# Kernel optimization log

Hardware: AMD Instinct MI355X
Metric: run time of the kernel (lower is better)

Reference implementation:

```python
import jax, jax.numpy as jnp
import numpy as np

P = 8  # patch size
EPS = 1e-5

def ln_ch(x, w, b):
    # WithBias LayerNorm over channel dim of (B,C,H,W): torch code flattens to (B,HW,C) and norms last dim
    mu = x.mean(axis=1, keepdims=True)
    var = ((x - mu) ** 2).mean(axis=1, keepdims=True)
    return (x - mu) / jnp.sqrt(var + EPS) * w[None, :, None, None] + b[None, :, None, None]

def conv1x1(x, w):
    # w: [C_out, C_in]
    return jnp.einsum('bchw,oc->bohw', x, w)

def dwconv3x3(x, w):
    # depthwise 3x3, w: [C,1,3,3]
    return jax.lax.conv_general_dilated(x, w, (1, 1), 'SAME', dimension_numbers=('NCHW', 'OIHW', 'NCHW'), feature_group_count=x.shape[1])

def patchify(x):
    b, c, H, W = x.shape
    return x.reshape(b, c, H // P, P, W // P, P).transpose(0, 1, 2, 4, 3, 5)  # b c h w p1 p2

def unpatchify(x):
    b, c, h, w, p1, p2 = x.shape
    return x.transpose(0, 1, 2, 4, 3, 5).reshape(b, c, h * p1, w * p2)

def setup_inputs() -> dict:
    key = jax.random.key(0)
    ks = jax.random.split(key, 16)
    B, C, H, W = 4, 64, 256, 256
    hid = 2 * C  # ffn_expansion_factor=2
    s = 0.02
    return {
        'x': jax.random.normal(ks[0], (B, C, H, W), jnp.float32),
        'evt': jax.random.normal(ks[1], (B, C, H, W), jnp.float32),
        'ln1i_w': jnp.ones((C,), jnp.float32), 'ln1i_b': jnp.zeros((C,), jnp.float32),
        'ln1e_w': jnp.ones((C,), jnp.float32), 'ln1e_b': jnp.zeros((C,), jnp.float32),
        'w_q': jax.random.normal(ks[2], (2 * C, C), jnp.float32) * s,
        'dw_q': jax.random.normal(ks[3], (2 * C, 1, 3, 3), jnp.float32) * s,
        'w_kv': jax.random.normal(ks[4], (4 * C, C), jnp.float32) * s,
        'dw_kv': jax.random.normal(ks[5], (4 * C, 1, 3, 3), jnp.float32) * s,
        'lnA_w': jnp.ones((2 * C,), jnp.float32), 'lnA_b': jnp.zeros((2 * C,), jnp.float32),
        'w_po_attn': jax.random.normal(ks[6], (C, 2 * C), jnp.float32) * s,
        'ln2_w': jnp.ones((C,), jnp.float32), 'ln2_b': jnp.zeros((C,), jnp.float32),
        'w_pi': jax.random.normal(ks[7], (2 * hid, C), jnp.float32) * s,
        'fft_param': jnp.ones((2 * hid, 1, 1, P, P // 2 + 1), jnp.float32),
        'dw_ffn': jax.random.normal(ks[8], (2 * hid, 1, 3, 3), jnp.float32) * s,
        'w_po_ffn': jax.random.normal(ks[9], (C, hid), jnp.float32) * s,
    }

def reference(x, evt, ln1i_w, ln1i_b, ln1e_w, ln1e_b, w_q, dw_q, w_kv, dw_kv, lnA_w, lnA_b, w_po_attn, ln2_w, ln2_b, w_pi, fft_param, dw_ffn, w_po_ffn):
    # ---- EventFSAS cross attention ----
    xn = ln_ch(x, ln1i_w, ln1i_b)
    en = ln_ch(evt, ln1e_w, ln1e_b)
    q = dwconv3x3(conv1x1(xn, w_q), dw_q)               # (B,2C,H,W)
    kv = dwconv3x3(conv1x1(en, w_kv), dw_kv)            # (B,4C,H,W)
    k, v = jnp.split(kv, 2, axis=1)
    qf = jnp.fft.rfft2(patchify(q))                      # (B,2C,h,w,8,5) complex
    kf = jnp.fft.rfft2(patchify(k))
    out = jnp.fft.irfft2(qf * kf, s=(P, P))
    out = ln_ch(unpatchify(out), lnA_w, lnA_b)
    x = x + conv1x1(v * out, w_po_attn)
    # ---- DFFN ----
    y = conv1x1(ln_ch(x, ln2_w, ln2_b), w_pi)            # (B,4C,H,W)
    yf = jnp.fft.rfft2(patchify(y)) * fft_param
    y = unpatchify(jnp.fft.irfft2(yf, s=(P, P)))
    y = dwconv3x3(y, dw_ffn)
    y1, y2 = jnp.split(y, 2, axis=1)
    y = jax.nn.gelu(y1, approximate=False) * y2          # torch nn.GELU is exact erf form
    return x + conv1x1(y, w_po_ffn)
```

## Files before the change

### kernel.cpp

```cpp
#include <hip/hip_runtime.h>

#define HW 65536
#define NPOS 262144

typedef unsigned int   u32;
typedef unsigned short u16;
typedef __attribute__((ext_vector_type(8))) short v8s;
typedef __attribute__((ext_vector_type(4))) float f32x4;
typedef __attribute__((ext_vector_type(2))) float f32x2;

__device__ __forceinline__ float bf2f(u16 h){
  union { u32 u; float f; } c; c.u = ((u32)h) << 16; return c.f;
}
__device__ __forceinline__ u16 f2bf(float f){
  union { u32 u; float f; } c; c.f = f;
  u32 r = c.u + 0x7fffu + ((c.u >> 16) & 1u);
  return (u16)(r >> 16);
}
__device__ __forceinline__ u32 pk2(float a, float b){
  return (u32)f2bf(a) | ((u32)f2bf(b) << 16);
}
__device__ __forceinline__ v8s as8(uint4 u){
  union { uint4 a; v8s b; } c; c.a = u; return c.b;
}
__device__ __forceinline__ f32x2 up2(u32 u){
  union { u32 u; float f; } lo, hi;
  lo.u = u << 16; hi.u = u & 0xffff0000u;
  f32x2 r; r.x = lo.f; r.y = hi.f; return r;
}
__device__ __forceinline__ float gelu_exact(float x){
  return 0.5f*x*(1.0f+erff(x*0.70710678118654752f));
}

__device__ void fold_w(const float* __restrict__ W, int rows,
                       const float* __restrict__ lw, const float* __restrict__ lb,
                       u16* __restrict__ Wf, float* __restrict__ A, float* __restrict__ B){
  int tid = threadIdx.x;
  for (int e = tid; e < rows*64; e += 256) Wf[e] = f2bf(lw[e & 63] * W[e]);
  for (int r = tid; r < rows; r += 256){
    float a = 0.f, b2 = 0.f;
    for (int c = 0; c < 64; c++){ float w = W[r*64+c]; a += lw[c]*w; b2 += lb[c]*w; }
    A[r] = a; B[r] = b2;
  }
}

__global__ void k_prep(const float* __restrict__ M, float* __restrict__ g,
    const float* wq,  const float* l1iw, const float* l1ib, u16* wqf,  float* aq,  float* bq,
    const float* wkv, const float* l1ew, const float* l1eb, u16* wkvf, float* akv, float* bkv,
    const float* wpi, const float* l2w,  const float* l2b,  u16* wpif, float* api, float* bpi,
    const float* wpa, u16* wpaf, const float* wpf, u16* wpff)
{
  int blk = blockIdx.x, tid = threadIdx.x;
  if (blk < 64){
    int t = blk*256 + tid;
    int c = t >> 6, uv = t & 63, u = uv >> 3, v = uv & 7;
    const float* mc = M + c*40;
    const float ctab[8] = {1.f, 0.70710678118654752f, 0.f, -0.70710678118654752f,
                           -1.f, -0.70710678118654752f, 0.f, 0.70710678118654752f};
    float acc = 0.f;
    for (int k1=0;k1<8;k1++)
      for (int k2=0;k2<8;k2++){
        float s = (k2<=4) ? mc[k1*5+k2] : mc[(((8-k1)&7)*5) + (8-k2)];
        acc += s * ctab[(k1*u + k2*v)&7];
      }
    g[t] = acc * (1.f/64.f);
  } else if (blk == 64){ fold_w(wq, 128, l1iw, l1ib, wqf, aq, bq); }
  else if (blk == 65){ fold_w(wkv, 256, l1ew, l1eb, wkvf, akv, bkv); }
  else if (blk == 66){ fold_w(wpi, 256, l2w, l2b, wpif, api, bpi); }
  else if (blk == 67){ for (int e=tid; e<64*128; e+=256) wpaf[e] = f2bf(wpa[e]); }
  else               { for (int e=tid; e<64*128; e+=256) wpff[e] = f2bf(wpf[e]); }
}

__global__ void k_prep2(const float* __restrict__ g, u16* __restrict__ CM){
  int c = blockIdx.x;
  const float* gc = g + (size_t)c*64;
  u16* cm = CM + (size_t)c*4096;
  for (int e = threadIdx.x; e < 4096; e += 256){
    int o = e >> 6, i = e & 63;
    int du = ((o>>3) - (i>>3)) & 7, dv = ((o&7) - (i&7)) & 7;
    cm[e] = f2bf(gc[du*8 + dv]);
  }
}

struct GA {
  const float* src; const u16* Wf; const float* Af; const float* Bf;
  u32* dst; int o0; int dstOffP; int Cdp; int b0; int pxbase;
};

template<int NZ>
__global__ __launch_bounds__(256) void k_gemm64(GA a0, GA a1){
  GA a = (blockIdx.y == 0) ? a0 : a1;
  __shared__ uint4 lsX[128*8];
  __shared__ uint4 lsW[64*NZ*8];
  __shared__ float2 sPart[256];
  __shared__ float2 sStat[128];
  int tid = threadIdx.x;
  int px = tid & 127, hf = tid >> 7;
  int p0 = a.pxbase + blockIdx.x*128;
  int b = p0 >> 16, hwb = p0 & 65535;
  {
    const uint4* wsrc = (const uint4*)(a.Wf + (size_t)a.o0*64);
    #pragma unroll
    for (int i=0; i<NZ*2; i++){
      int idx = i*256 + tid, row = idx>>3, s = idx&7;
      lsW[row*8 + (s ^ (row&7))] = wsrc[idx];
    }
  }
  {
    const float* sp = a.src + (size_t)b*64*HW + hwb + px + (size_t)(hf*32)*HW;
    float e[32];
    #pragma unroll
    for (int c=0;c<32;c++) e[c] = sp[(size_t)c*HW];
    float sm = 0.f, sq = 0.f;
    #pragma unroll
    for (int c=0;c<32;c++){ sm += e[c]; sq += e[c]*e[c]; }
    uint4* xrow = lsX + px*8;
    #pragma unroll
    for (int sl=0; sl<4; sl++){
      uint4 pkv;
      pkv.x = pk2(e[sl*8+0], e[sl*8+1]); pkv.y = pk2(e[sl*8+2], e[sl*8+3]);
      pkv.z = pk2(e[sl*8+4], e[sl*8+5]); pkv.w = pk2(e[sl*8+6], e[sl*8+7]);
      xrow[(hf*4+sl) ^ (px&7)] = pkv;
    }
    sPart[tid] = make_float2(sm, sq);
  }
  __syncthreads();
  if (tid < 128){
    float2 A = sPart[tid], B = sPart[tid+128];
    float s = A.x + B.x, q = A.y + B.y;
    float mu = s*(1.f/64.f);
    float var = q*(1.f/64.f) - mu*mu;
    sStat[tid] = make_float2(mu, rsqrtf(fmaxf(var,0.f)+1e-5f));
  }
  __syncthreads();
  int w = tid>>6, l = tid&63, g = l>>4, c15 = l&15;
  float2 stv[2];
  #pragma unroll
  for (int pp=0;pp<2;pp++) stv[pp] = sStat[w*32 + pp*16 + c15];

  #pragma unroll
  for (int z=0; z<NZ; z++){
    f32x4 acc[2][4];
    #pragma unroll
    for (int pp=0;pp<2;pp++)
      #pragma unroll
      for (int po=0;po<4;po++) acc[pp][po] = (f32x4){0.f,0.f,0.f,0.f};
    #pragma unroll
    for (int kk=0; kk<2; kk++){
      v8s wf[4], xf[2];
      #pragma unroll
      for (int po=0;po<4;po++){ int row = z*64 + po*16 + c15; wf[po] = as8(lsW[row*8 + ((kk*4+g) ^ (row&7))]); }
      #pragma unroll
      for (int pp=0;pp<2;pp++){ int row = w*32 + pp*16 + c15; xf[pp] = as8(lsX[row*8 + ((kk*4+g) ^ (row&7))]); }
      #pragma unroll
      for (int pp=0;pp<2;pp++)
        #pragma unroll
        for (int po=0;po<4;po++)
          acc[pp][po] = __builtin_amdgcn_mfma_f32_16x16x32_bf16(wf[po], xf[pp], acc[pp][po], 0,0,0);
    }
    size_t obaseP = ((size_t)(b - a.b0)*a.Cdp + a.dstOffP + z*32)*HW + hwb + w*32;
    #pragma unroll
    for (int po=0;po<4;po++)
      #pragma unroll
      for (int j2=0;j2<2;j2++){
        int oc = po*16 + g*4 + j2*2;
        float A0 = a.Af[a.o0 + z*64 + oc],   B0 = a.Bf[a.o0 + z*64 + oc];
        float A1 = a.Af[a.o0 + z*64 + oc+1], B1 = a.Bf[a.o0 + z*64 + oc+1];
        int ocp = po*8 + g*2 + j2;
        u32* dp = a.dst + obaseP + (size_t)ocp*HW + c15;
        #pragma unroll
        for (int pp=0;pp<2;pp++){
          float lo = stv[pp].y*(acc[pp][po][j2*2  ] - stv[pp].x*A0) + B0;
          float hi = stv[pp].y*(acc[pp][po][j2*2+1] - stv[pp].x*A1) + B1;
          dp[pp*16] = pk2(lo, hi);
        }
      }
  }
}

__global__ __launch_bounds__(256) void k_gemm_attn(
    const float* __restrict__ x, const u32* __restrict__ orawp, const u32* __restrict__ vbp,
    const float* __restrict__ lnw, const float* __restrict__ lnb,
    const u16* __restrict__ Wf, float* __restrict__ out)
{
  __shared__ uint4 lsX[128*16];
  __shared__ uint4 lsW[64*16];
  __shared__ float2 sPart[256];
  __shared__ float2 sStat[128];
  int tid = threadIdx.x;
  int p0 = blockIdx.x*128;
  int b = p0 >> 16, hwb = p0 & 65535;
  int px = tid & 127, hf = tid >> 7;
  {
    const uint4* wsrc = (const uint4*)Wf;
    #pragma unroll
    for (int i=0;i<4;i++){
      int idx = i*256 + tid, row = idx>>4, s = idx&15;
      lsW[row*16 + (s ^ (row&15))] = wsrc[idx];
    }
  }
  const u32* orp = orawp + ((size_t)b*64 + hf*32)*HW + hwb + px;
  {
    u32 r32[32];
    #pragma unroll
    for (int i=0;i<32;i++) r32[i] = orp[(size_t)i*HW];
    float sum = 0.f, ssq = 0.f;
    #pragma unroll
    for (int sl=0; sl<8; sl++){
      u32 wds[4];
      #pragma unroll
      for (int q2=0;q2<4;q2++){
        u32 wv = r32[sl*4+q2];
        float fl = bf2f((u16)(wv&0xffff)), fh = bf2f((u16)(wv>>16));
        sum += fl + fh; ssq += fl*fl + fh*fh;
        wds[q2] = wv;
      }
      int s = hf*8 + sl;
      lsX[px*16 + (s ^ (px&15))] = make_uint4(wds[0],wds[1],wds[2],wds[3]);
    }
    sPart[tid] = make_float2(sum, ssq);
  }
  __syncthreads();
  if (tid < 128){
    float2 A = sPart[tid], B = sPart[tid+128];
    float s = A.x + B.x, q = A.y + B.y;
    float mu = s*(1.f/128.f);
    float var = q*(1.f/128.f) - mu*mu;
    sStat[tid] = make_float2(mu, rsqrtf(fmaxf(var,0.f)+1e-5f));
  }
  __syncthreads();
  {
    float2 st = sStat[px];
    const u32* vp = vbp + ((size_t)b*64 + hf*32)*HW + hwb + px;
    u32 v32[32];
    #pragma unroll
    for (int i=0;i<32;i++) v32[i] = vp[(size_t)i*HW];
    #pragma unroll
    for (int sl=0; sl<8; sl++){
      int s = hf*8 + sl;
      int li = px*16 + (s ^ (px&15));
      uint4 raw = lsX[li];
      u32 wds[4] = {raw.x, raw.y, raw.z, raw.w};
      u32 ow[4];
      #pragma unroll
      for (int q2=0;q2<4;q2++){
        int ch = hf*64 + sl*8 + q2*2;
        float e0 = bf2f((u16)(wds[q2]&0xffff)), e1 = bf2f((u16)(wds[q2]>>16));
        u32 vv = v32[sl*4+q2];
        float v0 = bf2f((u16)(vv&0xffff)), v1 = bf2f((u16)(vv>>16));
        float r0 = ((e0-st.x)*st.y*lnw[ch  ] + lnb[ch  ])*v0;
        float r1 = ((e1-st.x)*st.y*lnw[ch+1] + lnb[ch+1])*v1;
        ow[q2] = pk2(r0, r1);
      }
      lsX[li] = make_uint4(ow[0],ow[1],ow[2],ow[3]);
    }
  }
  __syncthreads();
  int w4 = tid>>6, l = tid&63, g = l>>4, c15 = l&15;
  f32x4 acc[2][4];
  #pragma unroll
  for (int pp=0;pp<2;pp++)
    #pragma unroll
    for (int po=0;po<4;po++) acc[pp][po] = (f32x4){0.f,0.f,0.f,0.f};
  #pragma unroll
  for (int kk=0; kk<4; kk++){
    v8s wf[4], xf[2];
    #pragma unroll
    for (int po=0;po<4;po++){ int row = po*16 + c15; wf[po] = as8(lsW[row*16 + ((kk*4+g) ^ (row&15))]); }
    #pragma unroll
    for (int pp=0;pp<2;pp++){ int row = w4*32 + pp*16 + c15; xf[pp] = as8(lsX[row*16 + ((kk*4+g) ^ (row&15))]); }
    #pragma unroll
    for (int pp=0;pp<2;pp++)
      #pragma unroll
      for (int po=0;po<4;po++)
        acc[pp][po] = __builtin_amdgcn_mfma_f32_16x16x32_bf16(wf[po], xf[pp], acc[pp][po], 0,0,0);
  }
  size_t obase = (size_t)b*64*HW + hwb + w4*32;
  #pragma unroll
  for (int po=0;po<4;po++)
    #pragma unroll
    for (int j=0;j<4;j++){
      int oc = po*16 + g*4 + j;
      const float* xs = x + obase + (size_t)oc*HW + c15;
      float* dp = out + obase + (size_t)oc*HW + c15;
      #pragma unroll
      for (int pp=0;pp<2;pp++) dp[pp*16] = xs[pp*16] + acc[pp][po][j];
    }
}

__global__ __launch_bounds__(256) void k_gemm_ffn(
    const u32* __restrict__ y3gp, const u16* __restrict__ Wf, float* __restrict__ out,
    int pxbase, int b0)
{
  __shared__ uint4 lsX[128*16];
  __shared__ uint4 lsW[64*16];
  int tid = threadIdx.x;
  int p0 = pxbase + blockIdx.x*128;
  int b = p0 >> 16, hwb = p0 & 65535;
  int px = tid & 127, hf = tid >> 7;
  {
    const uint4* wsrc = (const uint4*)Wf;
    #pragma unroll
    for (int i=0;i<4;i++){
      int idx = i*256 + tid, row = idx>>4, s = idx&15;
      lsW[row*16 + (s ^ (row&15))] = wsrc[idx];
    }
  }
  const u32* yp = y3gp + ((size_t)(b-b0)*64 + hf*32)*HW + hwb + px;
  {
    u32 r32[32];
    #pragma unroll
    for (int i=0;i<32;i++) r32[i] = yp[(size_t)i*HW];
    #pragma unroll
    for (int sl=0; sl<8; sl++){
      int s = hf*8 + sl;
      lsX[px*16 + (s ^ (px&15))] = make_uint4(r32[sl*4+0],r32[sl*4+1],r32[sl*4+2],r32[sl*4+3]);
    }
  }
  __syncthreads();
  int w4 = tid>>6, l = tid&63, g = l>>4, c15 = l&15;
  f32x4 acc[2][4];
  #pragma unroll
  for (int pp=0;pp<2;pp++)
    #pragma unroll
    for (int po=0;po<4;po++) acc[pp][po] = (f32x4){0.f,0.f,0.f,0.f};
  #pragma unroll
  for (int kk=0; kk<4; kk++){
    v8s wf[4], xf[2];
    #pragma unroll
    for (int po=0;po<4;po++){ int row = po*16 + c15; wf[po] = as8(lsW[row*16 + ((kk*4+g) ^ (row&15))]); }
    #pragma unroll
    for (int pp=0;pp<2;pp++){ int row = w4*32 + pp*16 + c15; xf[pp] = as8(lsX[row*16 + ((kk*4+g) ^ (row&15))]); }
    #pragma unroll
    for (int pp=0;pp<2;pp++)
      #pragma unroll
      for (int po=0;po<4;po++)
        acc[pp][po] = __builtin_amdgcn_mfma_f32_16x16x32_bf16(wf[po], xf[pp], acc[pp][po], 0,0,0);
  }
  size_t obase = (size_t)b*64*HW + hwb + w4*32;
  #pragma unroll
  for (int po=0;po<4;po++)
    #pragma unroll
    for (int j=0;j<4;j++){
      int oc = po*16 + g*4 + j;
      float* dp = out + obase + (size_t)oc*HW + c15;
      #pragma unroll
      for (int pp=0;pp<2;pp++) dp[pp*16] = dp[pp*16] + acc[pp][po][j];
    }
}

__device__ __forceinline__ void dw8p_acc2(const u32* __restrict__ sp,
    const float* __restrict__ w9lo, const float* __restrict__ w9hi,
    int h, int w8, f32x2 a2[8])
{
  #pragma unroll
  for (int r=0;r<3;r++){
    int hh = h + r - 1;
    if (hh < 0 || hh > 255) continue;
    const u32* rp = sp + hh*256 + w8;
    uint4 ua = *(const uint4*)rp;
    uint4 ub = *(const uint4*)(rp+4);
    u32 e[8] = {ua.x,ua.y,ua.z,ua.w,ub.x,ub.y,ub.z,ub.w};
    u32 lef = (w8 > 0)   ? rp[-1] : 0u;
    u32 rig = (w8 < 248) ? rp[8]  : 0u;
    f32x2 vm[10];
    vm[0] = up2(lef);
    #pragma unroll
    for (int j=0;j<8;j++) vm[j+1] = up2(e[j]);
    vm[9] = up2(rig);
    f32x2 wa = {w9lo[r*3  ], w9hi[r*3  ]};
    f32x2 wb = {w9lo[r*3+1], w9hi[r*3+1]};
    f32x2 wc = {w9lo[r*3+2], w9hi[r*3+2]};
    #pragma unroll
    for (int j=0;j<8;j++)
      a2[j] += vm[j]*wa + vm[j+1]*wb + vm[j+2]*wc;
  }
}

__global__ __launch_bounds__(256) void k_dw8p(
    const u32* __restrict__ src, const float* __restrict__ wgt, int c0,
    u32* __restrict__ dstp, int dstOffP, int prMask, int prShift)
{
  int t = blockIdx.x*256 + threadIdx.x;
  int w8 = (t & 31)*8, h = (t>>5) & 255;
  int plane = t >> 13;
  int pr = plane & prMask, b = plane >> prShift;
  const u32* sp = src + (size_t)plane*HW;
  const float* w9 = wgt + (size_t)(c0 + 2*pr)*9;
  f32x2 a2[8];
  #pragma unroll
  for (int j=0;j<8;j++) a2[j] = (f32x2){0.f,0.f};
  dw8p_acc2(sp, w9, w9+9, h, w8, a2);
  u32* dp = dstp + ((size_t)(b*64 + dstOffP + pr))*HW + h*256 + w8;
  uint4 s0, s1;
  s0.x=pk2(a2[0].x,a2[0].y); s0.y=pk2(a2[1].x,a2[1].y); s0.z=pk2(a2[2].x,a2[2].y); s0.w=pk2(a2[3].x,a2[3].y);
  s1.x=pk2(a2[4].x,a2[4].y); s1.y=pk2(a2[5].x,a2[5].y); s1.z=pk2(a2[6].x,a2[6].y); s1.w=pk2(a2[7].x,a2[7].y);
  *(uint4*)dp = s0; *(uint4*)(dp+4) = s1;
}

__global__ __launch_bounds__(256) void k_dw8gp(
    const u32* __restrict__ Y0p, const float* __restrict__ wgt, u32* __restrict__ Y3gp)
{
  int t = blockIdx.x*256 + threadIdx.x;
  int w8 = (t & 31)*8, h = (t>>5) & 255;
  int pc = t >> 13;
  int pr = pc & 63, bl = pc >> 6;
  const u32* spA = Y0p + ((size_t)(bl*128 + pr))*HW;
  const u32* spG = Y0p + ((size_t)(bl*128 + 64 + pr))*HW;
  const float* w9a = wgt + (size_t)(2*pr)*9;
  const float* w9g = wgt + (size_t)(128 + 2*pr)*9;
  f32x2 aA[8], aG[8];
  #pragma unroll
  for (int j=0;j<8;j++){ aA[j] = (f32x2){0.f,0.f}; aG[j] = (f32x2){0.f,0.f}; }
  dw8p_acc2(spA, w9a, w9a+9, h, w8, aA);
  dw8p_acc2(spG, w9g, w9g+9, h, w8, aG);
  u32* dp = Y3gp + ((size_t)(bl*64 + pr))*HW + h*256 + w8;
  uint4 s0, s1;
  s0.x=pk2(gelu_exact(aA[0].x)*aG[0].x, gelu_exact(aA[0].y)*aG[0].y);
  s0.y=pk2(gelu_exact(aA[1].x)*aG[1].x, gelu_exact(aA[1].y)*aG[1].y);
  s0.z=pk2(gelu_exact(aA[2].x)*aG[2].x, gelu_exact(aA[2].y)*aG[2].y);
  s0.w=pk2(gelu_exact(aA[3].x)*aG[3].x, gelu_exact(aA[3].y)*aG[3].y);
  s1.x=pk2(gelu_exact(aA[4].x)*aG[4].x, gelu_exact(aA[4].y)*aG[4].y);
  s1.y=pk2(gelu_exact(aA[5].x)*aG[5].x, gelu_exact(aA[5].y)*aG[5].y);
  s1.z=pk2(gelu_exact(aA[6].x)*aG[6].x, gelu_exact(aA[6].y)*aG[6].y);
  s1.w=pk2(gelu_exact(aA[7].x)*aG[7].x, gelu_exact(aA[7].y)*aG[7].y);
  *(uint4*)dp = s0; *(uint4*)(dp+4) = s1;
}

__global__ __launch_bounds__(256) void k_circqk4(
    const u32* __restrict__ bq, const u32* __restrict__ bk,
    const float* __restrict__ dwq, const float* __restrict__ dwk, int c0,
    u32* __restrict__ orawp, int oprBase, int cpb)
{
  __shared__ f32x2 qd[8][288];
  __shared__ f32x2 kd[8][288];
  int tid = threadIdx.x;
  int p = tid & 31, i = tid >> 5;
  int pr = blockIdx.y, b = blockIdx.z;
  int h0 = blockIdx.x*8;
  const u32* qp = bq + ((size_t)(b*cpb+pr))*HW;
  const u32* kp = bk + ((size_t)(b*cpb+pr))*HW;
  const float* wq9 = dwq + (size_t)(c0 + 2*pr)*9;
  const float* wk9 = dwk + (size_t)(c0 + 2*pr)*9;
  {
    f32x2 a2[8];
    #pragma unroll
    for (int j=0;j<8;j++) a2[j] = (f32x2){0.f,0.f};
    dw8p_acc2(qp, wq9, wq9+9, h0+i, p*8, a2);
    #pragma unroll
    for (int j=0;j<8;j++) qd[i][p*9+j] = a2[j];
  }
  {
    f32x2 a2[8];
    #pragma unroll
    for (int j=0;j<8;j++) a2[j] = (f32x2){0.f,0.f};
    dw8p_acc2(kp, wk9, wk9+9, h0+i, p*8, a2);
    #pragma unroll
    for (int j=0;j<8;j++) kd[i][p*9+j] = a2[j];
  }
  __syncthreads();
  f32x2 o[8];
  #pragma unroll
  for (int j=0;j<8;j++) o[j] = (f32x2){0.f,0.f};
  #pragma unroll
  for (int u=0;u<8;u++){
    int ku = (i-u)&7;
    f32x2 qv[8], kr[8];
    #pragma unroll
    for (int v=0;v<8;v++) qv[v] = qd[u][p*9+v];
    #pragma unroll
    for (int e=0;e<8;e++) kr[e] = kd[ku][p*9+e];
    #pragma unroll
    for (int v=0;v<8;v++){
      f32x2 qq = qv[v];
      #pragma unroll
      for (int j=0;j<8;j++)
        o[j] += qq * kr[(j-v)&7];
    }
  }
  u32* op = orawp + ((size_t)(b*64 + oprBase + pr))*HW + (size_t)(h0+i)*256 + p*8;
  uint4 s0, s1;
  s0.x=pk2(o[0].x,o[0].y); s0.y=pk2(o[1].x,o[1].y); s0.z=pk2(o[2].x,o[2].y); s0.w=pk2(o[3].x,o[3].y);
  s1.x=pk2(o[4].x,o[4].y); s1.y=pk2(o[5].x,o[5].y); s1.z=pk2(o[6].x,o[6].y); s1.w=pk2(o[7].x,o[7].y);
  *(uint4*)op = s0; *(uint4*)(op+4) = s1;
}

__global__ __launch_bounds__(256) void k_circg_mfma(
    u32* __restrict__ y, const u16* __restrict__ CM)
{
  __shared__ uint4 lsA[2][64*8];
  __shared__ uint4 lsB[2][64*8];
  int tid = threadIdx.x;
  int pr = blockIdx.y, b = blockIdx.z;
  int h0 = blockIdx.x*16;
  u32* plane = y + ((size_t)(b*128+pr))*HW;
  {
    const uint4* cmsrc = (const uint4*)(CM + (size_t)(2*pr)*4096);
    #pragma unroll
    for (int t=0; t<4; t++){
      int idx = t*256 + tid;
      int ch = idx >> 9, e = idx & 511;
      int row = e >> 3, s = e & 7;
      lsA[ch][row*8 + (s ^ (row&7))] = cmsrc[ch*512 + e];
    }
  }
  {
    #pragma unroll
    for (int t=0; t<2; t++){
      int rr = t*256 + tid;
      int n = rr >> 3, i = rr & 7;
      const u32* rp = plane + (size_t)(h0 + (n>>5)*8 + i)*256 + (n&31)*8;
      uint4 ua = *(const uint4*)rp;
      uint4 ub = *(const uint4*)(rp+4);
      u32 e[8] = {ua.x,ua.y,ua.z,ua.w,ub.x,ub.y,ub.z,ub.w};
      uint4 L, H;
      L.x = (e[0]&0xffffu) | (e[1]<<16);
      L.y = (e[2]&0xffffu) | (e[3]<<16);
      L.z = (e[4]&0xffffu) | (e[5]<<16);
      L.w = (e[6]&0xffffu) | (e[7]<<16);
      H.x = (e[0]>>16) | (e[1]&0xffff0000u);
      H.y = (e[2]>>16) | (e[3]&0xffff0000u);
      H.z = (e[4]>>16) | (e[5]&0xffff0000u);
      H.w = (e[6]>>16) | (e[7]&0xffff0000u);
      lsB[0][n*8 + (i ^ (n&7))] = L;
      lsB[1][n*8 + (i ^ (n&7))] = H;
    }
  }
  __syncthreads();
  int w = tid>>6, l = tid&63, g = l>>4, c15 = l&15;
  f32x4 acc[2][4];
  #pragma unroll
  for (int ch=0;ch<2;ch++)
    #pragma unroll
    for (int po=0;po<4;po++) acc[ch][po] = (f32x4){0.f,0.f,0.f,0.f};
  #pragma unroll
  for (int kk=0; kk<2; kk++){
    v8s bfr[2];
    { int row = w*16 + c15;
      bfr[0] = as8(lsB[0][row*8 + ((kk*4+g) ^ (row&7))]);
      bfr[1] = as8(lsB[1][row*8 + ((kk*4+g) ^ (row&7))]); }
    #pragma unroll
    for (int po=0;po<4;po++){
      int row = po*16 + c15;
      v8s aL = as8(lsA[0][row*8 + ((kk*4+g) ^ (row&7))]);
      v8s aH = as8(lsA[1][row*8 + ((kk*4+g) ^ (row&7))]);
      acc[0][po] = __builtin_amdgcn_mfma_f32_16x16x32_bf16(aL, bfr[0], acc[0][po], 0,0,0);
      acc[1][po] = __builtin_amdgcn_mfma_f32_16x16x32_bf16(aH, bfr[1], acc[1][po], 0,0,0);
    }
  }
  int patch = w*16 + c15;
  u32* pbase = plane + (size_t)(h0 + (patch>>5)*8)*256 + (patch&31)*8;
  #pragma unroll
  for (int po=0;po<4;po++){
    int oh = po*2 + (g>>1), ow4 = 4*(g&1);
    uint4 sv;
    sv.x = pk2(acc[0][po][0], acc[1][po][0]);
    sv.y = pk2(acc[0][po][1], acc[1][po][1]);
    sv.z = pk2(acc[0][po][2], acc[1][po][2]);
    sv.w = pk2(acc[0][po][3], acc[1][po][3]);
    *(uint4*)(pbase + (size_t)oh*256 + ow4) = sv;
  }
}

extern "C" void kernel_launch(void* const* d_in, const int* in_sizes, int n_in,
                              void* d_out, int out_size, void* d_ws, size_t ws_size,
                              hipStream_t stream)
{
  const float* x       = (const float*)d_in[0];
  const float* evt     = (const float*)d_in[1];
  const float* ln1i_w  = (const float*)d_in[2];
  const float* ln1i_b  = (const float*)d_in[3];
  const float* ln1e_w  = (const float*)d_in[4];
  const float* ln1e_b  = (const float*)d_in[5];
  const float* w_q     = (const float*)d_in[6];
  const float* dw_q    = (const float*)d_in[7];
  const float* w_kv    = (const float*)d_in[8];
  const float* dw_kv   = (const float*)d_in[9];
  const float* lnA_w   = (const float*)d_in[10];
  const float* lnA_b   = (const float*)d_in[11];
  const float* w_po_at = (const float*)d_in[12];
  const float* ln2_w   = (const float*)d_in[13];
  const float* ln2_b   = (const float*)d_in[14];
  const float* w_pi    = (const float*)d_in[15];
  const float* fft_par = (const float*)d_in[16];
  const float* dw_ffn  = (const float*)d_in[17];
  const float* w_poffn = (const float*)d_in[18];
  float* out = (float*)d_out;

  char* ws = (char*)d_ws;
  const size_t MiB = 1048576ull;
  bool big = (ws_size >= 200*MiB);
  size_t smOff = big ? 192*MiB : 160*MiB;
  char* sm = ws + smOff;
  float* G    = (float*)(sm);
  u16* WQF    = (u16*)(sm + 65536);
  u16* WKVF   = (u16*)(sm + 81920);
  u16* WPIF   = (u16*)(sm + 114688);
  u16* WPAF   = (u16*)(sm + 147456);
  u16* WPFF   = (u16*)(sm + 163840);
  float* AQ   = (float*)(sm + 180224);
  float* BQ   = (float*)(sm + 180736);
  float* AKV  = (float*)(sm + 181248);
  float* BKV  = (float*)(sm + 182272);
  float* API  = (float*)(sm + 183296);
  float* BPI  = (float*)(sm + 184320);
  u16* CMAT   = (u16*)(sm + 1*MiB);

  dim3 blk256(256);

  k_prep<<<69, blk256, 0, stream>>>(fft_par, G,
      w_q, ln1i_w, ln1i_b, WQF, AQ, BQ,
      w_kv, ln1e_w, ln1e_b, WKVF, AKV, BKV,
      w_pi, ln2_w, ln2_b, WPIF, API, BPI,
      w_po_at, WPAF, w_poffn, WPFF);
  k_prep2<<<256, blk256, 0, stream>>>(G, CMAT);

  if (big){
    u32* QBUF  = (u32*)(ws);
    u32* KBUF  = (u32*)(ws + 64*MiB);
    u32* ORAWp = (u32*)(ws + 128*MiB);
    u32* PV    = (u32*)(ws + 64*MiB);
    u32* VBUFp = (u32*)(ws);
    u32* Y0p   = (u32*)(ws);
    u32* Y3Gp  = (u32*)(ws + 128*MiB);

    GA qa = {x,   WQF,  AQ,  BQ,  QBUF, 0, 0, 64, 0, 0};
    GA ka = {evt, WKVF, AKV, BKV, KBUF, 0, 0, 64, 0, 0};
    k_gemm64<2><<<dim3(2048,2,1), blk256, 0, stream>>>(qa, ka);
    k_circqk4<<<dim3(32,64,4), blk256, 0, stream>>>(QBUF, KBUF, dw_q, dw_kv, 0, ORAWp, 0, 64);
    GA va = {evt, WKVF, AKV, BKV, PV, 128, 0, 64, 0, 0};
    k_gemm64<2><<<dim3(2048,1,1), blk256, 0, stream>>>(va, va);
    k_dw8p<<<8192, blk256, 0, stream>>>(PV, dw_kv, 128, VBUFp, 0, 63, 6);
    k_gemm_attn<<<2048, blk256, 0, stream>>>(x, ORAWp, VBUFp, lnA_w, lnA_b, WPAF, out);
    GA pa = {out, WPIF, API, BPI, Y0p, 0, 0, 128, 0, 0};
    k_gemm64<4><<<dim3(2048,1,1), blk256, 0, stream>>>(pa, pa);
    k_circg_mfma<<<dim3(16,128,4), blk256, 0, stream>>>(Y0p, CMAT);
    k_dw8gp<<<8192, blk256, 0, stream>>>(Y0p, dw_ffn, Y3Gp);
    k_gemm_ffn<<<2048, blk256, 0, stream>>>(Y3Gp, WPFF, out, 0, 0);
  } else {
    u32* P1p   = (u32*)(ws);
    u32* ORAWp = (u32*)(ws + 32*MiB);
    u32* P2p   = (u32*)(ws + 96*MiB);
    u32* VBUFp = (u32*)(ws + 96*MiB);
    u32* Y0p   = (u32*)(ws);
    u32* Y3Gp  = (u32*)(ws + 64*MiB);

    for (int i=0;i<2;i++){
      GA qa = {x,   WQF,  AQ,  BQ,  P1p, 64*i, 0, 32, 0, 0};
      GA ka = {evt, WKVF, AKV, BKV, P2p, 64*i, 0, 32, 0, 0};
      k_gemm64<1><<<dim3(2048,2,1), blk256, 0, stream>>>(qa, ka);
      k_circqk4<<<dim3(32,32,4), blk256, 0, stream>>>(P1p, P2p, dw_q, dw_kv, 64*i, ORAWp, 32*i, 32);
    }
    for (int i=0;i<2;i++){
      GA va = {evt, WKVF, AKV, BKV, P1p, 128+64*i, 0, 32, 0, 0};
      k_gemm64<1><<<dim3(2048,1,1), blk256, 0, stream>>>(va, va);
      k_dw8p<<<4096, blk256, 0, stream>>>(P1p, dw_kv, 128+64*i, VBUFp, 32*i, 31, 5);
    }
    k_gemm_attn<<<2048, blk256, 0, stream>>>(x, ORAWp, VBUFp, lnA_w, lnA_b, WPAF, out);
    for (int h=0;h<2;h++){
      GA pa = {out, WPIF, API, BPI, Y0p, 0, 0, 128, 2*h, h*131072};
      k_gemm64<4><<<dim3(1024,1,1), blk256, 0, stream>>>(pa, pa);
      k_circg_mfma<<<dim3(16,128,2), blk256, 0, stream>>>(Y0p, CMAT);
      k_dw8gp<<<4096, blk256, 0, stream>>>(Y0p, dw_ffn, Y3Gp);
      k_gemm_ffn<<<1024, blk256, 0, stream>>>(Y3Gp, WPFF, out, h*131072, 2*h);
    }
  }
}
```

Baseline: 462.4 us.

## Fuse V-projection GEMM with circular QK kernel into one heterogeneous launch

Merges the V 1x1-conv GEMM and the per-patch circular Q·K correlation into a single kernel, where one block in five runs the GEMM and the rest run the circulant work. The V projection output is staged in the output buffer so it no longer aliases the K buffer that the circulant blocks are still reading. The aim is to overlap the memory-bound GEMM with the compute-heavy circulant work and remove one launch plus the tail bubble between them. It also adds stride parameters to the dwconv and circqk kernels, and in exchange brings branch-divergent block roles and a shared-memory footprint sized for the larger path.

```diff
diff --git a/kernel.cpp b/kernel.cpp
--- a/kernel.cpp
+++ b/kernel.cpp
@@ -178,177 +178,6 @@
   }
 }
 
-__global__ __launch_bounds__(256) void k_gemm_attn(
-    const float* __restrict__ x, const u32* __restrict__ orawp, const u32* __restrict__ vbp,
-    const float* __restrict__ lnw, const float* __restrict__ lnb,
-    const u16* __restrict__ Wf, float* __restrict__ out)
-{
-  __shared__ uint4 lsX[128*16];
-  __shared__ uint4 lsW[64*16];
-  __shared__ float2 sPart[256];
-  __shared__ float2 sStat[128];
-  int tid = threadIdx.x;
-  int p0 = blockIdx.x*128;
-  int b = p0 >> 16, hwb = p0 & 65535;
-  int px = tid & 127, hf = tid >> 7;
-  {
-    const uint4* wsrc = (const uint4*)Wf;
-    #pragma unroll
-    for (int i=0;i<4;i++){
-      int idx = i*256 + tid, row = idx>>4, s = idx&15;
-      lsW[row*16 + (s ^ (row&15))] = wsrc[idx];
-    }
-  }
-  const u32* orp = orawp + ((size_t)b*64 + hf*32)*HW + hwb + px;
-  {
-    u32 r32[32];
-    #pragma unroll
-    for (int i=0;i<32;i++) r32[i] = orp[(size_t)i*HW];
-    float sum = 0.f, ssq = 0.f;
-    #pragma unroll
-    for (int sl=0; sl<8; sl++){
-      u32 wds[4];
-      #pragma unroll
-      for (int q2=0;q2<4;q2++){
-        u32 wv = r32[sl*4+q2];
-        float fl = bf2f((u16)(wv&0xffff)), fh = bf2f((u16)(wv>>16));
-        sum += fl + fh; ssq += fl*fl + fh*fh;
-        wds[q2] = wv;
-      }
-      int s = hf*8 + sl;
-      lsX[px*16 + (s ^ (px&15))] = make_uint4(wds[0],wds[1],wds[2],wds[3]);
-    }
-    sPart[tid] = make_float2(sum, ssq);
-  }
-  __syncthreads();
-  if (tid < 128){
-    float2 A = sPart[tid], B = sPart[tid+128];
-    float s = A.x + B.x, q = A.y + B.y;
-    float mu = s*(1.f/128.f);
-    float var = q*(1.f/128.f) - mu*mu;
-    sStat[tid] = make_float2(mu, rsqrtf(fmaxf(var,0.f)+1e-5f));
-  }
-  __syncthreads();
-  {
-    float2 st = sStat[px];
-    const u32* vp = vbp + ((size_t)b*64 + hf*32)*HW + hwb + px;
-    u32 v32[32];
-    #pragma unroll
-    for (int i=0;i<32;i++) v32[i] = vp[(size_t)i*HW];
-    #pragma unroll
-    for (int sl=0; sl<8; sl++){
-      int s = hf*8 + sl;
-      int li = px*16 + (s ^ (px&15));
-      uint4 raw = lsX[li];
-      u32 wds[4] = {raw.x, raw.y, raw.z, raw.w};
-      u32 ow[4];
-      #pragma unroll
-      for (int q2=0;q2<4;q2++){
-        int ch = hf*64 + sl*8 + q2*2;
-        float e0 = bf2f((u16)(wds[q2]&0xffff)), e1 = bf2f((u16)(wds[q2]>>16));
-        u32 vv = v32[sl*4+q2];
-        float v0 = bf2f((u16)(vv&0xffff)), v1 = bf2f((u16)(vv>>16));
-        float r0 = ((e0-st.x)*st.y*lnw[ch  ] + lnb[ch  ])*v0;
-        float r1 = ((e1-st.x)*st.y*lnw[ch+1] + lnb[ch+1])*v1;
-        ow[q2] = pk2(r0, r1);
-      }
-      lsX[li] = make_uint4(ow[0],ow[1],ow[2],ow[3]);
-    }
-  }
-  __syncthreads();
-  int w4 = tid>>6, l = tid&63, g = l>>4, c15 = l&15;
-  f32x4 acc[2][4];
-  #pragma unroll
-  for (int pp=0;pp<2;pp++)
-    #pragma unroll
-    for (int po=0;po<4;po++) acc[pp][po] = (f32x4){0.f,0.f,0.f,0.f};
-  #pragma unroll
-  for (int kk=0; kk<4; kk++){
-    v8s wf[4], xf[2];
-    #pragma unroll
-    for (int po=0;po<4;po++){ int row = po*16 + c15; wf[po] = as8(lsW[row*16 + ((kk*4+g) ^ (row&15))]); }
-    #pragma unroll
-    for (int pp=0;pp<2;pp++){ int row = w4*32 + pp*16 + c15; xf[pp] = as8(lsX[row*16 + ((kk*4+g) ^ (row&15))]); }
-    #pragma unroll
-    for (int pp=0;pp<2;pp++)
-      #pragma unroll
-      for (int po=0;po<4;po++)
-        acc[pp][po] = __builtin_amdgcn_mfma_f32_16x16x32_bf16(wf[po], xf[pp], acc[pp][po], 0,0,0);
-  }
-  size_t obase = (size_t)b*64*HW + hwb + w4*32;
-  #pragma unroll
-  for (int po=0;po<4;po++)
-    #pragma unroll
-    for (int j=0;j<4;j++){
-      int oc = po*16 + g*4 + j;
-      const float* xs = x + obase + (size_t)oc*HW + c15;
-      float* dp = out + obase + (size_t)oc*HW + c15;
-      #pragma unroll
-      for (int pp=0;pp<2;pp++) dp[pp*16] = xs[pp*16] + acc[pp][po][j];
-    }
-}
-
-__global__ __launch_bounds__(256) void k_gemm_ffn(
-    const u32* __restrict__ y3gp, const u16* __restrict__ Wf, float* __restrict__ out,
-    int pxbase, int b0)
-{
-  __shared__ uint4 lsX[128*16];
-  __shared__ uint4 lsW[64*16];
-  int tid = threadIdx.x;
-  int p0 = pxbase + blockIdx.x*128;
-  int b = p0 >> 16, hwb = p0 & 65535;
-  int px = tid & 127, hf = tid >> 7;
-  {
-    const uint4* wsrc = (const uint4*)Wf;
-    #pragma unroll
-    for (int i=0;i<4;i++){
-      int idx = i*256 + tid, row = idx>>4, s = idx&15;
-      lsW[row*16 + (s ^ (row&15))] = wsrc[idx];
-    }
-  }
-  const u32* yp = y3gp + ((size_t)(b-b0)*64 + hf*32)*HW + hwb + px;
-  {
-    u32 r32[32];
-    #pragma unroll
-    for (int i=0;i<32;i++) r32[i] = yp[(size_t)i*HW];
-    #pragma unroll
-    for (int sl=0; sl<8; sl++){
-      int s = hf*8 + sl;
-      lsX[px*16 + (s ^ (px&15))] = make_uint4(r32[sl*4+0],r32[sl*4+1],r32[sl*4+2],r32[sl*4+3]);
-    }
-  }
-  __syncthreads();
-  int w4 = tid>>6, l = tid&63, g = l>>4, c15 = l&15;
-  f32x4 acc[2][4];
-  #pragma unroll
-  for (int pp=0;pp<2;pp++)
-    #pragma unroll
-    for (int po=0;po<4;po++) acc[pp][po] = (f32x4){0.f,0.f,0.f,0.f};
-  #pragma unroll
-  for (int kk=0; kk<4; kk++){
-    v8s wf[4], xf[2];
-    #pragma unroll
-    for (int po=0;po<4;po++){ int row = po*16 + c15; wf[po] = as8(lsW[row*16 + ((kk*4+g) ^ (row&15))]); }
-    #pragma unroll
-    for (int pp=0;pp<2;pp++){ int row = w4*32 + pp*16 + c15; xf[pp] = as8(lsX[row*16 + ((kk*4+g) ^ (row&15))]); }
-    #pragma unroll
-    for (int pp=0;pp<2;pp++)
-      #pragma unroll
-      for (int po=0;po<4;po++)
-        acc[pp][po] = __builtin_amdgcn_mfma_f32_16x16x32_bf16(wf[po], xf[pp], acc[pp][po], 0,0,0);
-  }
-  size_t obase = (size_t)b*64*HW + hwb + w4*32;
-  #pragma unroll
-  for (int po=0;po<4;po++)
-    #pragma unroll
-    for (int j=0;j<4;j++){
-      int oc = po*16 + g*4 + j;
-      float* dp = out + obase + (size_t)oc*HW + c15;
-      #pragma unroll
-      for (int pp=0;pp<2;pp++) dp[pp*16] = dp[pp*16] + acc[pp][po][j];
-    }
-}
-
 __device__ __forceinline__ void dw8p_acc2(const u32* __restrict__ sp,
     const float* __restrict__ w9lo, const float* __restrict__ w9hi,
     int h, int w8, f32x2 a2[8])
@@ -377,15 +206,338 @@
   }
 }
 
+__global__ __launch_bounds__(256) void k_fused_cv(
+    const u32* __restrict__ bq, const u32* __restrict__ bk,
+    const float* __restrict__ dwq, const float* __restrict__ dwk,
+    u32* __restrict__ orawp,
+    const float* __restrict__ vsrc, const u16* __restrict__ Wf,
+    const float* __restrict__ Af, const float* __restrict__ Bf,
+    u32* __restrict__ vdst)
+{
+  __shared__ uint4 smemq[2304];
+  int bid = blockIdx.x;
+  int tid = threadIdx.x;
+  if (bid % 5 == 0){
+    int gb = bid / 5;
+    uint4* lsX = smemq;
+    uint4* lsW = smemq + 1024;
+    float2* sPart = (float2*)(smemq + 2048);
+    float2* sStat = (float2*)((char*)(smemq + 2048) + 2048);
+    int px = tid & 127, hf = tid >> 7;
+    int p0 = gb*128;
+    int b = p0 >> 16, hwb = p0 & 65535;
+    {
+      const uint4* wsrc = (const uint4*)(Wf + (size_t)128*64);
+      #pragma unroll
+      for (int i=0; i<4; i++){
+        int idx = i*256 + tid, row = idx>>3, s = idx&7;
+        lsW[row*8 + (s ^ (row&7))] = wsrc[idx];
+      }
+    }
+    {
+      const float* sp = vsrc + (size_t)b*64*HW + hwb + px + (size_t)(hf*32)*HW;
+      float e[32];
+      #pragma unroll
+      for (int c=0;c<32;c++) e[c] = sp[(size_t)c*HW];
+      float sm = 0.f, sq = 0.f;
+      #pragma unroll
+      for (int c=0;c<32;c++){ sm += e[c]; sq += e[c]*e[c]; }
+      uint4* xrow = lsX + px*8;
+      #pragma unroll
+      for (int sl=0; sl<4; sl++){
+        uint4 pkv;
+        pkv.x = pk2(e[sl*8+0], e[sl*8+1]); pkv.y = pk2(e[sl*8+2], e[sl*8+3]);
+        pkv.z = pk2(e[sl*8+4], e[sl*8+5]); pkv.w = pk2(e[sl*8+6], e[sl*8+7]);
+        xrow[(hf*4+sl) ^ (px&7)] = pkv;
+      }
+      sPart[tid] = make_float2(sm, sq);
+    }
+    __syncthreads();
+    if (tid < 128){
+      float2 A = sPart[tid], B = sPart[tid+128];
+      float s = A.x + B.x, q = A.y + B.y;
+      float mu = s*(1.f/64.f);
+      float var = q*(1.f/64.f) - mu*mu;
+      sStat[tid] = make_float2(mu, rsqrtf(fmaxf(var,0.f)+1e-5f));
+    }
+    __syncthreads();
+    int w = tid>>6, l = tid&63, g = l>>4, c15 = l&15;
+    float2 stv[2];
+    #pragma unroll
+    for (int pp=0;pp<2;pp++) stv[pp] = sStat[w*32 + pp*16 + c15];
+    #pragma unroll
+    for (int z=0; z<2; z++){
+      f32x4 acc[2][4];
+      #pragma unroll
+      for (int pp=0;pp<2;pp++)
+        #pragma unroll
+        for (int po=0;po<4;po++) acc[pp][po] = (f32x4){0.f,0.f,0.f,0.f};
+      #pragma unroll
+      for (int kk=0; kk<2; kk++){
+        v8s wf[4], xf[2];
+        #pragma unroll
+        for (int po=0;po<4;po++){ int row = z*64 + po*16 + c15; wf[po] = as8(lsW[row*8 + ((kk*4+g) ^ (row&7))]); }
+        #pragma unroll
+        for (int pp=0;pp<2;pp++){ int row = w*32 + pp*16 + c15; xf[pp] = as8(lsX[row*8 + ((kk*4+g) ^ (row&7))]); }
+        #pragma unroll
+        for (int pp=0;pp<2;pp++)
+          #pragma unroll
+          for (int po=0;po<4;po++)
+            acc[pp][po] = __builtin_amdgcn_mfma_f32_16x16x32_bf16(wf[po], xf[pp], acc[pp][po], 0,0,0);
+      }
+      size_t obaseP = ((size_t)b*64 + z*32)*HW + hwb + w*32;
+      #pragma unroll
+      for (int po=0;po<4;po++)
+        #pragma unroll
+        for (int j2=0;j2<2;j2++){
+          int oc = po*16 + g*4 + j2*2;
+          float A0 = Af[128 + z*64 + oc],   B0 = Bf[128 + z*64 + oc];
+          float A1 = Af[128 + z*64 + oc+1], B1 = Bf[128 + z*64 + oc+1];
+          int ocp = po*8 + g*2 + j2;
+          u32* dp = vdst + obaseP + (size_t)ocp*HW + c15;
+          #pragma unroll
+          for (int pp=0;pp<2;pp++){
+            float lo = stv[pp].y*(acc[pp][po][j2*2  ] - stv[pp].x*A0) + B0;
+            float hi = stv[pp].y*(acc[pp][po][j2*2+1] - stv[pp].x*A1) + B1;
+            dp[pp*16] = pk2(lo, hi);
+          }
+        }
+    }
+  } else {
+    int cq = bid - bid/5 - 1;
+    int strip = cq & 31, pr = (cq >> 5) & 63, b = cq >> 11;
+    f32x2 (*qd)[288] = (f32x2(*)[288])smemq;
+    f32x2 (*kd)[288] = (f32x2(*)[288])((char*)smemq + 18432);
+    int p = tid & 31, i = tid >> 5;
+    int h0 = strip*8;
+    const u32* qp = bq + ((size_t)(b*64+pr))*HW;
+    const u32* kp = bk + ((size_t)(b*64+pr))*HW;
+    const float* wq9 = dwq + (size_t)(2*pr)*9;
+    const float* wk9 = dwk + (size_t)(2*pr)*9;
+    {
+      f32x2 a2[8];
+      #pragma unroll
+      for (int j=0;j<8;j++) a2[j] = (f32x2){0.f,0.f};
+      dw8p_acc2(qp, wq9, wq9+9, h0+i, p*8, a2);
+      #pragma unroll
+      for (int j=0;j<8;j++) qd[i][p*9+j] = a2[j];
+    }
+    {
+      f32x2 a2[8];
+      #pragma unroll
+      for (int j=0;j<8;j++) a2[j] = (f32x2){0.f,0.f};
+      dw8p_acc2(kp, wk9, wk9+9, h0+i, p*8, a2);
+      #pragma unroll
+      for (int j=0;j<8;j++) kd[i][p*9+j] = a2[j];
+    }
+    __syncthreads();
+    f32x2 o[8];
+    #pragma unroll
+    for (int j=0;j<8;j++) o[j] = (f32x2){0.f,0.f};
+    #pragma unroll
+    for (int u=0;u<8;u++){
+      int ku = (i-u)&7;
+      f32x2 qv[8], kr[8];
+      #pragma unroll
+      for (int v=0;v<8;v++) qv[v] = qd[u][p*9+v];
+      #pragma unroll
+      for (int e=0;e<8;e++) kr[e] = kd[ku][p*9+e];
+      #pragma unroll
+      for (int v=0;v<8;v++){
+        f32x2 qq = qv[v];
+        #pragma unroll
+        for (int j=0;j<8;j++)
+          o[j] += qq * kr[(j-v)&7];
+      }
+    }
+    u32* op = orawp + ((size_t)(b*64 + pr))*HW + (size_t)(h0+i)*256 + p*8;
+    uint4 s0, s1;
+    s0.x=pk2(o[0].x,o[0].y); s0.y=pk2(o[1].x,o[1].y); s0.z=pk2(o[2].x,o[2].y); s0.w=pk2(o[3].x,o[3].y);
+    s1.x=pk2(o[4].x,o[4].y); s1.y=pk2(o[5].x,o[5].y); s1.z=pk2(o[6].x,o[6].y); s1.w=pk2(o[7].x,o[7].y);
+    *(uint4*)op = s0; *(uint4*)(op+4) = s1;
+  }
+}
+
+__global__ __launch_bounds__(256) void k_gemm_attn(
+    const float* __restrict__ x, const u32* __restrict__ orawp, const u32* __restrict__ vbp,
+    const float* __restrict__ lnw, const float* __restrict__ lnb,
+    const u16* __restrict__ Wf, float* __restrict__ out)
+{
+  __shared__ uint4 lsX[128*16];
+  __shared__ uint4 lsW[64*16];
+  __shared__ float2 sPart[256];
+  __shared__ float2 sStat[128];
+  int tid = threadIdx.x;
+  int p0 = blockIdx.x*128;
+  int b = p0 >> 16, hwb = p0 & 65535;
+  int px = tid & 127, hf = tid >> 7;
+  {
+    const uint4* wsrc = (const uint4*)Wf;
+    #pragma unroll
+    for (int i=0;i<4;i++){
+      int idx = i*256 + tid, row = idx>>4, s = idx&15;
+      lsW[row*16 + (s ^ (row&15))] = wsrc[idx];
+    }
+  }
+  const u32* orp = orawp + ((size_t)b*64 + hf*32)*HW + hwb + px;
+  {
+    u32 r32[32];
+    #pragma unroll
+    for (int i=0;i<32;i++) r32[i] = orp[(size_t)i*HW];
+    float sum = 0.f, ssq = 0.f;
+    #pragma unroll
+    for (int sl=0; sl<8; sl++){
+      u32 wds[4];
+      #pragma unroll
+      for (int q2=0;q2<4;q2++){
+        u32 wv = r32[sl*4+q2];
+        float fl = bf2f((u16)(wv&0xffff)), fh = bf2f((u16)(wv>>16));
+        sum += fl + fh; ssq += fl*fl + fh*fh;
+        wds[q2] = wv;
+      }
+      int s = hf*8 + sl;
+      lsX[px*16 + (s ^ (px&15))] = make_uint4(wds[0],wds[1],wds[2],wds[3]);
+    }
+    sPart[tid] = make_float2(sum, ssq);
+  }
+  __syncthreads();
+  if (tid < 128){
+    float2 A = sPart[tid], B = sPart[tid+128];
+    float s = A.x + B.x, q = A.y + B.y;
+    float mu = s*(1.f/128.f);
+    float var = q*(1.f/128.f) - mu*mu;
+    sStat[tid] = make_float2(mu, rsqrtf(fmaxf(var,0.f)+1e-5f));
+  }
+  __syncthreads();
+  {
+    float2 st = sStat[px];
+    const u32* vp = vbp + ((size_t)b*64 + hf*32)*HW + hwb + px;
+    u32 v32[32];
+    #pragma unroll
+    for (int i=0;i<32;i++) v32[i] = vp[(size_t)i*HW];
+    #pragma unroll
+    for (int sl=0; sl<8; sl++){
+      int s = hf*8 + sl;
+      int li = px*16 + (s ^ (px&15));
+      uint4 raw = lsX[li];
+      u32 wds[4] = {raw.x, raw.y, raw.z, raw.w};
+      u32 ow[4];
+      #pragma unroll
+      for (int q2=0;q2<4;q2++){
+        int ch = hf*64 + sl*8 + q2*2;
+        float e0 = bf2f((u16)(wds[q2]&0xffff)), e1 = bf2f((u16)(wds[q2]>>16));
+        u32 vv = v32[sl*4+q2];
+        float v0 = bf2f((u16)(vv&0xffff)), v1 = bf2f((u16)(vv>>16));
+        float r0 = ((e0-st.x)*st.y*lnw[ch  ] + lnb[ch  ])*v0;
+        float r1 = ((e1-st.x)*st.y*lnw[ch+1] + lnb[ch+1])*v1;
+        ow[q2] = pk2(r0, r1);
+      }
+      lsX[li] = make_uint4(ow[0],ow[1],ow[2],ow[3]);
+    }
+  }
+  __syncthreads();
+  int w4 = tid>>6, l = tid&63, g = l>>4, c15 = l&15;
+  f32x4 acc[2][4];
+  #pragma unroll
+  for (int pp=0;pp<2;pp++)
+    #pragma unroll
+    for (int po=0;po<4;po++) acc[pp][po] = (f32x4){0.f,0.f,0.f,0.f};
+  #pragma unroll
+  for (int kk=0; kk<4; kk++){
+    v8s wf[4], xf[2];
+    #pragma unroll
+    for (int po=0;po<4;po++){ int row = po*16 + c15; wf[po] = as8(lsW[row*16 + ((kk*4+g) ^ (row&15))]); }
+    #pragma unroll
+    for (int pp=0;pp<2;pp++){ int row = w4*32 + pp*16 + c15; xf[pp] = as8(lsX[row*16 + ((kk*4+g) ^ (row&15))]); }
+    #pragma unroll
+    for (int pp=0;pp<2;pp++)
+      #pragma unroll
+      for (int po=0;po<4;po++)
+        acc[pp][po] = __builtin_amdgcn_mfma_f32_16x16x32_bf16(wf[po], xf[pp], acc[pp][po], 0,0,0);
+  }
+  size_t obase = (size_t)b*64*HW + hwb + w4*32;
+  #pragma unroll
+  for (int po=0;po<4;po++)
+    #pragma unroll
+    for (int j=0;j<4;j++){
+      int oc = po*16 + g*4 + j;
+      const float* xs = x + obase + (size_t)oc*HW + c15;
+      float* dp = out + obase + (size_t)oc*HW + c15;
+      #pragma unroll
+      for (int pp=0;pp<2;pp++) dp[pp*16] = xs[pp*16] + acc[pp][po][j];
+    }
+}
+
+__global__ __launch_bounds__(256) void k_gemm_ffn(
+    const u32* __restrict__ y3gp, const u16* __restrict__ Wf, float* __restrict__ out,
+    int pxbase, int b0)
+{
+  __shared__ uint4 lsX[128*16];
+  __shared__ uint4 lsW[64*16];
+  int tid = threadIdx.x;
+  int p0 = pxbase + blockIdx.x*128;
+  int b = p0 >> 16, hwb = p0 & 65535;
+  int px = tid & 127, hf = tid >> 7;
+  {
+    const uint4* wsrc = (const uint4*)Wf;
+    #pragma unroll
+    for (int i=0;i<4;i++){
+      int idx = i*256 + tid, row = idx>>4, s = idx&15;
+      lsW[row*16 + (s ^ (row&15))] = wsrc[idx];
+    }
+  }
+  const u32* yp = y3gp + ((size_t)(b-b0)*64 + hf*32)*HW + hwb + px;
+  {
+    u32 r32[32];
+    #pragma unroll
+    for (int i=0;i<32;i++) r32[i] = yp[(size_t)i*HW];
+    #pragma unroll
+    for (int sl=0; sl<8; sl++){
+      int s = hf*8 + sl;
+      lsX[px*16 + (s ^ (px&15))] = make_uint4(r32[sl*4+0],r32[sl*4+1],r32[sl*4+2],r32[sl*4+3]);
+    }
+  }
+  __syncthreads();
+  int w4 = tid>>6, l = tid&63, g = l>>4, c15 = l&15;
+  f32x4 acc[2][4];
+  #pragma unroll
+  for (int pp=0;pp<2;pp++)
+    #pragma unroll
+    for (int po=0;po<4;po++) acc[pp][po] = (f32x4){0.f,0.f,0.f,0.f};
+  #pragma unroll
+  for (int kk=0; kk<4; kk++){
+    v8s wf[4], xf[2];
+    #pragma unroll
+    for (int po=0;po<4;po++){ int row = po*16 + c15; wf[po] = as8(lsW[row*16 + ((kk*4+g) ^ (row&15))]); }
+    #pragma unroll
+    for (int pp=0;pp<2;pp++){ int row = w4*32 + pp*16 + c15; xf[pp] = as8(lsX[row*16 + ((kk*4+g) ^ (row&15))]); }
+    #pragma unroll
+    for (int pp=0;pp<2;pp++)
+      #pragma unroll
+      for (int po=0;po<4;po++)
+        acc[pp][po] = __builtin_amdgcn_mfma_f32_16x16x32_bf16(wf[po], xf[pp], acc[pp][po], 0,0,0);
+  }
+  size_t obase = (size_t)b*64*HW + hwb + w4*32;
+  #pragma unroll
+  for (int po=0;po<4;po++)
+    #pragma unroll
+    for (int j=0;j<4;j++){
+      int oc = po*16 + g*4 + j;
+      float* dp = out + obase + (size_t)oc*HW + c15;
+      #pragma unroll
+      for (int pp=0;pp<2;pp++) dp[pp*16] = dp[pp*16] + acc[pp][po][j];
+    }
+}
+
 __global__ __launch_bounds__(256) void k_dw8p(
     const u32* __restrict__ src, const float* __restrict__ wgt, int c0,
-    u32* __restrict__ dstp, int dstOffP, int prMask, int prShift)
+    u32* __restrict__ dstp, int dstOffP, int prMask, int prShift, int srcStride, int srcBase)
 {
   int t = blockIdx.x*256 + threadIdx.x;
   int w8 = (t & 31)*8, h = (t>>5) & 255;
   int plane = t >> 13;
   int pr = plane & prMask, b = plane >> prShift;
-  const u32* sp = src + (size_t)plane*HW;
+  const u32* sp = src + ((size_t)(b*srcStride + srcBase + pr))*HW;
   const float* w9 = wgt + (size_t)(c0 + 2*pr)*9;
   f32x2 a2[8];
   #pragma unroll
@@ -430,7 +582,7 @@
 __global__ __launch_bounds__(256) void k_circqk4(
     const u32* __restrict__ bq, const u32* __restrict__ bk,
     const float* __restrict__ dwq, const float* __restrict__ dwk, int c0,
-    u32* __restrict__ orawp, int oprBase, int cpb)
+    u32* __restrict__ orawp, int oprBase, int cpbq, int cpbk)
 {
   __shared__ f32x2 qd[8][288];
   __shared__ f32x2 kd[8][288];
@@ -438,8 +590,8 @@
   int p = tid & 31, i = tid >> 5;
   int pr = blockIdx.y, b = blockIdx.z;
   int h0 = blockIdx.x*8;
-  const u32* qp = bq + ((size_t)(b*cpb+pr))*HW;
-  const u32* kp = bk + ((size_t)(b*cpb+pr))*HW;
+  const u32* qp = bq + ((size_t)(b*cpbq+pr))*HW;
+  const u32* kp = bk + ((size_t)(b*cpbk+pr))*HW;
   const float* wq9 = dwq + (size_t)(c0 + 2*pr)*9;
   const float* wk9 = dwk + (size_t)(c0 + 2*pr)*9;
   {
@@ -619,18 +771,17 @@
     u32* QBUF  = (u32*)(ws);
     u32* KBUF  = (u32*)(ws + 64*MiB);
     u32* ORAWp = (u32*)(ws + 128*MiB);
-    u32* PV    = (u32*)(ws + 64*MiB);
     u32* VBUFp = (u32*)(ws);
     u32* Y0p   = (u32*)(ws);
     u32* Y3Gp  = (u32*)(ws + 128*MiB);
+    u32* PV    = (u32*)out;
 
     GA qa = {x,   WQF,  AQ,  BQ,  QBUF, 0, 0, 64, 0, 0};
     GA ka = {evt, WKVF, AKV, BKV, KBUF, 0, 0, 64, 0, 0};
     k_gemm64<2><<<dim3(2048,2,1), blk256, 0, stream>>>(qa, ka);
-    k_circqk4<<<dim3(32,64,4), blk256, 0, stream>>>(QBUF, KBUF, dw_q, dw_kv, 0, ORAWp, 0, 64);
-    GA va = {evt, WKVF, AKV, BKV, PV, 128, 0, 64, 0, 0};
-    k_gemm64<2><<<dim3(2048,1,1), blk256, 0, stream>>>(va, va);
-    k_dw8p<<<8192, blk256, 0, stream>>>(PV, dw_kv, 128, VBUFp, 0, 63, 6);
+    k_fused_cv<<<10240, blk256, 0, stream>>>(QBUF, KBUF, dw_q, dw_kv, ORAWp,
+                                             evt, WKVF, AKV, BKV, PV);
+    k_dw8p<<<8192, blk256, 0, stream>>>(PV, dw_kv, 128, VBUFp, 0, 63, 6, 64, 0);
     k_gemm_attn<<<2048, blk256, 0, stream>>>(x, ORAWp, VBUFp, lnA_w, lnA_b, WPAF, out);
     GA pa = {out, WPIF, API, BPI, Y0p, 0, 0, 128, 0, 0};
     k_gemm64<4><<<dim3(2048,1,1), blk256, 0, stream>>>(pa, pa);
@@ -649,12 +800,12 @@
       GA qa = {x,   WQF,  AQ,  BQ,  P1p, 64*i, 0, 32, 0, 0};
       GA ka = {evt, WKVF, AKV, BKV, P2p, 64*i, 0, 32, 0, 0};
       k_gemm64<1><<<dim3(2048,2,1), blk256, 0, stream>>>(qa, ka);
-      k_circqk4<<<dim3(32,32,4), blk256, 0, stream>>>(P1p, P2p, dw_q, dw_kv, 64*i, ORAWp, 32*i, 32);
+      k_circqk4<<<dim3(32,32,4), blk256, 0, stream>>>(P1p, P2p, dw_q, dw_kv, 64*i, ORAWp, 32*i, 32, 32);
     }
     for (int i=0;i<2;i++){
       GA va = {evt, WKVF, AKV, BKV, P1p, 128+64*i, 0, 32, 0, 0};
       k_gemm64<1><<<dim3(2048,1,1), blk256, 0, stream>>>(va, va);
-      k_dw8p<<<4096, blk256, 0, stream>>>(P1p, dw_kv, 128+64*i, VBUFp, 32*i, 31, 5);
+      k_dw8p<<<4096, blk256, 0, stream>>>(P1p, dw_kv, 128+64*i, VBUFp, 32*i, 31, 5, 32, 0);
     }
     k_gemm_attn<<<2048, blk256, 0, stream>>>(x, ORAWp, VBUFp, lnA_w, lnA_b, WPAF, out);
     for (int h=0;h<2;h++){
```

Measured after the change: 509.5 us. +10.2%, slower.
